# Optimization experiments

Measured on AMD Instinct MI355X. Metric: run time of the kernel, lower is better.

Reference implementation:

```python
import jax, jax.numpy as jnp
import numpy as np

B, N1, N2, D, L, H = 2, 384, 384, 128, 3, 128
DM_MIN = 0.5


def _gat_layer(x, adj, W, Wb, A, gW, gb):
    # GAT_gate from jaechanglim/DTI_PDBbind: attention softmax over dim 1, gated residual
    h = x @ W + Wb                                   # [B,N,D]
    e = jnp.einsum('bjl,bkl->bjk', h @ A, h)
    e = e + jnp.swapaxes(e, 1, 2)
    att = jnp.where(adj > 0, e, -9e15)
    att = jax.nn.softmax(att, axis=1) * adj
    h_prime = jax.nn.relu(jnp.einsum('bij,bjk->bik', att, h))
    coeff = jax.nn.sigmoid(jnp.concatenate([x, h_prime], -1) @ gW + gb)  # [B,N,1]
    return coeff * x + (1.0 - coeff) * h_prime


def _pair_mlp(h1g, h2g, W1, b1, W2, b2):
    # MLP(concat(h1_i, h2_j)) without materializing the [B,N1,N2,2D] concat:
    # split W1 into ligand / protein halves and broadcast-add the projections.
    p1 = jnp.einsum('bnd,dk->bnk', h1g, W1[:D])      # [B,N1,H]
    p2 = jnp.einsum('bmd,dk->bmk', h2g, W1[D:])      # [B,N2,H]
    hid = jax.nn.relu(p1[:, :, None, :] + p2[:, None, :, :] + b1)  # [B,N1,N2,H]
    return (hid @ W2 + b2)[..., 0]                   # [B,N1,N2]


def reference(h1, adj1, h2, dmv, charge1, charge2, vdw_epsilon, vdw_sigma,
              delta_uff, valid1, valid2, no_metal1, no_metal2,
              node_W, gat_W, gat_Wb, gat_A, gat_gW, gat_gb,
              pair_W1, pair_b1, pair_W2, pair_b2,
              vdw_coeff, duff_coeff, int_W1, int_b1, int_W2, int_b2):
    h1g = h1 @ node_W
    h2g = h2 @ node_W
    for i in range(L):  # only ligand graph is convolved (as in the source)
        h1g = _gat_layer(h1g, adj1, gat_W[i], gat_Wb[i], gat_A[i], gat_gW[i], gat_gb[i])

    dm = jnp.sqrt(jnp.sum(dmv * dmv, -1) + 1e-10)    # [B,N1,N2]
    dm = jnp.where(dm < DM_MIN, 1e10, dm)

    # coulomb term (pair MLPs 0,1)
    cA = jax.nn.sigmoid(_pair_mlp(h1g, h2g, pair_W1[0], pair_b1[0], pair_W2[0], pair_b2[0]))
    cN = jax.nn.sigmoid(_pair_mlp(h1g, h2g, pair_W1[1], pair_b1[1], pair_W2[1], pair_b2[1])) * 2.0 + 1.0
    charge12 = charge1[:, :, None] * charge2[:, None, :]
    e_c = cA * charge12 * jnp.power(1.0 / dm, cN)
    e_c = e_c * valid1[:, :, None] * valid2[:, None, :]
    e_c = jnp.clip(e_c, -100.0, 100.0)
    e_c = jnp.sum(e_c, axis=(1, 2))[:, None]

    # vdw term (pair MLPs 2=A sigmoid, 3=B tanh, 4=N sigmoid)
    vA = (jax.nn.sigmoid(_pair_mlp(h1g, h2g, pair_W1[2], pair_b1[2], pair_W2[2], pair_b2[2])) * 0.6 + 0.7)
    vA = vA * (vdw_coeff[0] * vdw_coeff[0]) * vdw_epsilon
    vB = jnp.tanh(_pair_mlp(h1g, h2g, pair_W1[3], pair_b1[3], pair_W2[3], pair_b2[3])) * 0.6 + 0.7
    vN = jax.nn.sigmoid(_pair_mlp(h1g, h2g, pair_W1[4], pair_b1[4], pair_W2[4], pair_b2[4])) * 2.0 + 5.0
    dm0 = vdw_sigma * vB
    dm0 = jnp.where(dm0 < 1e-4, 1.0, dm0)
    r = jnp.power(dm0 / dm, vN)
    e_v = vA * (r * r - 2.0 * r)                     # (dm0/dm)^(2N) - 2(dm0/dm)^N
    e_v = e_v * no_metal1[:, :, None] * no_metal2[:, None, :]
    e_v = jnp.minimum(e_v, 100.0)
    e_v = jnp.sum(e_v, axis=(1, 2))[:, None]

    # conformational energy difference term
    e_u = (duff_coeff[0] * duff_coeff[0] * delta_uff)[:, None]

    # learned intercept from pooled ligand features
    hs = jnp.sum(h1g * valid1[..., None], axis=1)
    inter = jax.nn.relu(hs @ int_W1 + int_b1) @ int_W2 + int_b2

    return jnp.concatenate([e_c, e_v, e_u, inter], -1)  # [B,4]


def setup_inputs() -> dict:
    key = jax.random.key(0)
    ks = jax.random.split(key, 24)
    inp = {}
    inp['h1'] = jax.random.normal(ks[0], (B, N1, 54), jnp.float32)
    inp['h2'] = jax.random.normal(ks[1], (B, N2, 54), jnp.float32)
    a = jax.random.uniform(ks[2], (B, N1, N1))
    adj = (a > 0.9).astype(jnp.float32)
    adj = jnp.maximum(adj, jnp.swapaxes(adj, 1, 2))
    inp['adj1'] = jnp.maximum(adj, jnp.eye(N1, dtype=jnp.float32)[None])
    inp['dmv'] = jax.random.normal(ks[3], (B, N1, N2, 3), jnp.float32) * 3.0
    inp['charge1'] = jax.random.normal(ks[4], (B, N1), jnp.float32) * 0.3
    inp['charge2'] = jax.random.normal(ks[5], (B, N2), jnp.float32) * 0.3
    inp['vdw_epsilon'] = jax.random.uniform(ks[6], (B, N1, N2), jnp.float32) * 0.3
    inp['vdw_sigma'] = 3.0 + jax.random.uniform(ks[7], (B, N1, N2), jnp.float32)
    inp['delta_uff'] = jax.random.uniform(ks[8], (B,), jnp.float32) * 5.0
    inp['valid1'] = jnp.ones((B, N1), jnp.float32)
    inp['valid2'] = jnp.ones((B, N2), jnp.float32)
    inp['no_metal1'] = jnp.ones((B, N1), jnp.float32)
    inp['no_metal2'] = jnp.ones((B, N2), jnp.float32)
    # parameters
    inp['node_W'] = jax.random.normal(ks[9], (54, D), jnp.float32) * 0.1
    inp['gat_W'] = jax.random.normal(ks[10], (L, D, D), jnp.float32) * (1.0 / np.sqrt(D))
    inp['gat_Wb'] = jnp.zeros((L, D), jnp.float32)
    inp['gat_A'] = jax.random.normal(ks[11], (L, D, D), jnp.float32) * 0.05
    inp['gat_gW'] = jax.random.normal(ks[12], (L, 2 * D, 1), jnp.float32) * 0.05
    inp['gat_gb'] = jnp.zeros((L, 1), jnp.float32)
    inp['pair_W1'] = jax.random.normal(ks[13], (5, 2 * D, H), jnp.float32) * 0.05
    inp['pair_b1'] = jnp.zeros((5, H), jnp.float32)
    inp['pair_W2'] = jax.random.normal(ks[14], (5, H, 1), jnp.float32) * 0.1
    inp['pair_b2'] = jnp.zeros((5, 1), jnp.float32)
    inp['vdw_coeff'] = jnp.array([0.02], jnp.float32)
    inp['duff_coeff'] = jnp.array([0.1], jnp.float32)
    inp['int_W1'] = jax.random.normal(ks[15], (D, H), jnp.float32) * 0.05
    inp['int_b1'] = jnp.zeros((H,), jnp.float32)
    inp['int_W2'] = jax.random.normal(ks[16], (H, 1), jnp.float32) * 0.1
    inp['int_b2'] = jnp.zeros((1,), jnp.float32)
    return inp
```

## Files before the change

### kernel.cpp

```cpp
#include <hip/hip_runtime.h>
#include <math.h>

#define BB 2
#define NN 384
#define DD 128
#define HH 128
#define RT_ALL (BB * NN)
#define PCOLS (BB * NN)

__device__ __forceinline__ float sigmoidf_(float x) { return 1.f / (1.f + __expf(-x)); }
__device__ __forceinline__ float tanhf_(float x)    { return 1.f - 2.f / (__expf(2.f * x) + 1.f); }

__global__ __launch_bounds__(256) void k_embed(
    const float* __restrict__ h1, const float* __restrict__ h2,
    const float* __restrict__ nW, float* __restrict__ h1g, float* __restrict__ h2g) {
  int r0 = blockIdx.x * 2;
  int tid = threadIdx.x;
  const float* src; float* dst; int rb;
  if (r0 < RT_ALL) { src = h1; dst = h1g; rb = r0; }
  else             { src = h2; dst = h2g; rb = r0 - RT_ALL; }
  __shared__ float xs[2][54];
  if (tid < 108) xs[tid / 54][tid % 54] = src[rb * 54 + tid];
  __syncthreads();
  int rr = tid >> 7, c = tid & 127;
  float acc = 0.f;
#pragma unroll 6
  for (int k = 0; k < 54; ++k) acc += xs[rr][k] * nW[k * DD + c];
  dst[(rb + rr) * DD + c] = acc;
}

__global__ __launch_bounds__(256) void k_gat_hhA(
    const float* __restrict__ x, const float* __restrict__ W,
    const float* __restrict__ Wb, const float* __restrict__ A,
    float* __restrict__ h, float* __restrict__ hA,
    float* __restrict__ hT, float* __restrict__ hAT) {
  int r = blockIdx.x;
  int tid = threadIdx.x, c = tid & 127, kh = tid >> 7;
  __shared__ float xs[DD], hs[DD];
  __shared__ float ph[2][DD];
  if (tid < DD) xs[tid] = x[r * DD + tid];
  __syncthreads();
  float acc = 0.f;
  const float* Wp = W + (kh * 64) * DD + c;
#pragma unroll 4
  for (int k = 0; k < 64; ++k) acc += xs[kh * 64 + k] * Wp[k * DD];
  ph[kh][c] = acc;
  __syncthreads();
  if (tid < DD) {
    float hv = ph[0][tid] + ph[1][tid] + Wb[tid];
    h[r * DD + tid] = hv; hT[tid * PCOLS + r] = hv; hs[tid] = hv;
  }
  __syncthreads();
  acc = 0.f;
  const float* Ap = A + (kh * 64) * DD + c;
#pragma unroll 4
  for (int k = 0; k < 64; ++k) acc += hs[kh * 64 + k] * Ap[k * DD];
  ph[kh][c] = acc;
  __syncthreads();
  if (tid < DD) {
    float av = ph[0][tid] + ph[1][tid];
    hA[r * DD + tid] = av; hAT[tid * PCOLS + r] = av;
  }
}

__global__ __launch_bounds__(384) void k_gat_att(
    const float* __restrict__ h, const float* __restrict__ hA,
    const float* __restrict__ hT, const float* __restrict__ hAT,
    const float* __restrict__ adj, float* __restrict__ attT) {
  int col = blockIdx.x;
  int b = col / NN;
  int tid = threadIdx.x;
  const float* hrow  = h  + col * DD;
  const float* hArow = hA + col * DD;
  const float* hTb  = hT  + b * NN + tid;
  const float* hATb = hAT + b * NN + tid;
  float e = 0.f;
#pragma unroll 8
  for (int c = 0; c < DD; ++c)
    e += hATb[c * PCOLS] * hrow[c] + hTb[c * PCOLS] * hArow[c];
  float a = adj[col * NN + tid];
  __shared__ float rmx[6], rsm[6];
  float lmax = (a > 0.f) ? e : -3e38f;
#pragma unroll
  for (int off = 32; off > 0; off >>= 1) lmax = fmaxf(lmax, __shfl_down(lmax, off));
  if ((tid & 63) == 0) rmx[tid >> 6] = lmax;
  __syncthreads();
  float m = fmaxf(fmaxf(fmaxf(rmx[0], rmx[1]), fmaxf(rmx[2], rmx[3])), fmaxf(rmx[4], rmx[5]));
  float v = (a > 0.f) ? __expf(e - m) : 0.f;
  float s = v;
#pragma unroll
  for (int off = 32; off > 0; off >>= 1) s += __shfl_down(s, off);
  if ((tid & 63) == 0) rsm[tid >> 6] = s;
  __syncthreads();
  float inv = 1.f / (rsm[0] + rsm[1] + rsm[2] + rsm[3] + rsm[4] + rsm[5]);
  attT[col * NN + tid] = v * a * inv;
}

__global__ __launch_bounds__(256) void k_gat_out(
    const float* __restrict__ x, const float* __restrict__ h,
    const float* __restrict__ attT, const float* __restrict__ gW,
    const float* __restrict__ gb, float* __restrict__ out) {
  int r = blockIdx.x;
  int b = r / NN, i = r - b * NN;
  int tid = threadIdx.x, c = tid & 127, jh = tid >> 7;
  __shared__ float arow[NN];
  __shared__ float ph[2][DD];
  __shared__ float redw[2];
  for (int idx = tid; idx < NN; idx += 256) arow[idx] = attT[(b * NN + idx) * NN + i];
  __syncthreads();
  float acc = 0.f;
  const float* hp = h + (b * NN + jh * 192) * DD + c;
#pragma unroll 4
  for (int jj = 0; jj < 192; ++jj) acc += arow[jh * 192 + jj] * hp[jj * DD];
  ph[jh][c] = acc;
  __syncthreads();
  if (tid < DD) {
    float hpr = fmaxf(ph[0][tid] + ph[1][tid], 0.f);
    float xr = x[r * DD + tid];
    float v = xr * gW[tid] + hpr * gW[DD + tid];
#pragma unroll
    for (int off = 32; off > 0; off >>= 1) v += __shfl_down(v, off);
    if ((tid & 63) == 0) redw[tid >> 6] = v;
  }
  __syncthreads();
  if (tid < DD) {
    float hpr = fmaxf(ph[0][tid] + ph[1][tid], 0.f);
    float xr = x[r * DD + tid];
    float coeff = sigmoidf_(redw[0] + redw[1] + gb[0]);
    out[r * DD + tid] = coeff * xr + (1.f - coeff) * hpr;
  }
}

__global__ __launch_bounds__(256) void k_pair_proj(
    const float* __restrict__ h1g, const float* __restrict__ h2g,
    const float* __restrict__ W1, const float* __restrict__ b1,
    const float* __restrict__ delta_uff, const float* __restrict__ duff_coeff,
    float* __restrict__ p1, float* __restrict__ p2T, float* __restrict__ out) {
  const int RT = 16;
  int m = blockIdx.x % 5;
  int r0 = (blockIdx.x / 5) * RT;
  int tid = threadIdx.x, c = tid & 127, kh = tid >> 7;
  if (blockIdx.x == 0 && tid < BB * 4) {
    int bb = tid >> 2, cc = tid & 3;
    out[tid] = (cc == 2) ? duff_coeff[0] * duff_coeff[0] * delta_uff[bb] : 0.f;
  }
  bool lig = (r0 < RT_ALL);
  const float* src = lig ? h1g : h2g;
  int rb = lig ? r0 : r0 - RT_ALL;
  const float* W = W1 + (m * 256 + (lig ? 0 : 128)) * HH;
  __shared__ float xs[RT][DD];
  __shared__ float ps[RT][DD];
  for (int idx = tid; idx < RT * DD; idx += 256) xs[idx >> 7][idx & 127] = src[rb * DD + idx];
  __syncthreads();
  float acc[RT];
#pragma unroll
  for (int r = 0; r < RT; ++r) acc[r] = 0.f;
  const float* Wp = W + (kh * 64) * HH + c;
#pragma unroll 2
  for (int k = 0; k < 64; ++k) {
    float w = Wp[k * HH];
#pragma unroll
    for (int r = 0; r < RT; ++r) acc[r] += xs[r][kh * 64 + k] * w;
  }
  if (kh == 1) {
#pragma unroll
    for (int r = 0; r < RT; ++r) ps[r][c] = acc[r];
  }
  __syncthreads();
  if (kh == 0) {
    if (lig) {
      float bias = b1[m * HH + c];
#pragma unroll
      for (int r = 0; r < RT; ++r)
        p1[((rb + r) * 5 + m) * HH + c] = acc[r] + ps[r][c] + bias;
    } else {
      float* dst = p2T + (m * HH + c) * PCOLS + rb;
#pragma unroll
      for (int q = 0; q < RT / 4; ++q) {
        float4 v = make_float4(acc[4 * q + 0] + ps[4 * q + 0][c],
                               acc[4 * q + 1] + ps[4 * q + 1][c],
                               acc[4 * q + 2] + ps[4 * q + 2][c],
                               acc[4 * q + 3] + ps[4 * q + 3][c]);
        *(float4*)(dst + 4 * q) = v;
      }
    }
  }
}

__global__ __launch_bounds__(192) void k_pair_energy(
    const float* __restrict__ p1, const float* __restrict__ p2T,
    const float* __restrict__ W2, const float* __restrict__ b2,
    const float* __restrict__ dmv, const float* __restrict__ charge1,
    const float* __restrict__ charge2, const float* __restrict__ veps,
    const float* __restrict__ vsig, const float* __restrict__ valid1,
    const float* __restrict__ valid2, const float* __restrict__ nm1,
    const float* __restrict__ nm2, const float* __restrict__ vdw_coeff,
    const float* __restrict__ h1g, float* __restrict__ ws_int,
    float* __restrict__ out) {
  int tid = threadIdx.x;
  if (blockIdx.x >= 768) {
    int eb = blockIdx.x - 768;
    int b = eb >> 2, ch = eb & 3;
    if (tid < DD) {
      float acc = 0.f;
      int i0 = ch * 96;
#pragma unroll 4
      for (int i = 0; i < 96; ++i) {
        int gi = b * NN + i0 + i;
        acc += h1g[gi * DD + tid] * valid1[gi];
      }
      ws_int[eb * DD + tid] = acc;
    }
    return;
  }
  const int TI = 2;
  int tile = blockIdx.x >> 1, jh = blockIdx.x & 1;
  int r0 = tile * TI;
  int b = r0 / NN;
  int j = jh * 192 + tid;
  int col = b * NN + j;

  const float* q0 = p1 + (r0 + 0) * 5 * HH;
  const float* q1 = p1 + (r0 + 1) * 5 * HH;
  float acc0[5], acc1[5];
#pragma unroll
  for (int m = 0; m < 5; ++m) {
    const float* p2c = p2T + m * HH * PCOLS + col;
    const float* w2m = W2 + m * HH;
    const float* x0 = q0 + m * HH;
    const float* x1 = q1 + m * HH;
    float a0 = b2[m], a1 = b2[m];
#pragma unroll 8
    for (int h = 0; h < HH; ++h) {
      float pv = p2c[h * PCOLS];
      float w = w2m[h];
      a0 += fmaxf(x0[h] + pv, 0.f) * w;
      a1 += fmaxf(x1[h] + pv, 0.f) * w;
    }
    acc0[m] = a0; acc1[m] = a1;
  }

  float q2c = charge2[col], v2 = valid2[col], n2 = nm2[col];
  float vc2 = vdw_coeff[0] * vdw_coeff[0];
  float ec_sum = 0.f, ev_sum = 0.f;
#pragma unroll
  for (int ti = 0; ti < TI; ++ti) {
    const float* am = ti ? acc1 : acc0;
    int gi = r0 + ti;
    int pidx = gi * NN + j;
    float dx = dmv[pidx * 3 + 0], dy = dmv[pidx * 3 + 1], dz = dmv[pidx * 3 + 2];
    float dm = sqrtf(dx * dx + dy * dy + dz * dz + 1e-10f);
    if (dm < 0.5f) dm = 1e10f;
    float cA = sigmoidf_(am[0]);
    float cN = sigmoidf_(am[1]) * 2.f + 1.f;
    float e_c = cA * charge1[gi] * q2c * __powf(1.f / dm, cN);
    e_c *= valid1[gi] * v2;
    e_c = fminf(fmaxf(e_c, -100.f), 100.f);
    ec_sum += e_c;
    float vA = (sigmoidf_(am[2]) * 0.6f + 0.7f) * vc2 * veps[pidx];
    float vB = tanhf_(am[3]) * 0.6f + 0.7f;
    float vN = sigmoidf_(am[4]) * 2.f + 5.f;
    float dm0 = vsig[pidx] * vB;
    if (dm0 < 1e-4f) dm0 = 1.f;
    float rr = __powf(dm0 / dm, vN);
    float e_v = vA * (rr * rr - 2.f * rr);
    e_v *= nm1[gi] * n2;
    e_v = fminf(e_v, 100.f);
    ev_sum += e_v;
  }
#pragma unroll
  for (int off = 32; off > 0; off >>= 1) {
    ec_sum += __shfl_down(ec_sum, off);
    ev_sum += __shfl_down(ev_sum, off);
  }
  __shared__ float rec[3], rev[3];
  if ((tid & 63) == 0) { rec[tid >> 6] = ec_sum; rev[tid >> 6] = ev_sum; }
  __syncthreads();
  if (tid == 0) {
    atomicAdd(&out[b * 4 + 0], rec[0] + rec[1] + rec[2]);
    atomicAdd(&out[b * 4 + 1], rev[0] + rev[1] + rev[2]);
  }
}

__global__ __launch_bounds__(256) void k_intercept_fin(
    const float* __restrict__ ws_int, const float* __restrict__ W1,
    const float* __restrict__ b1, const float* __restrict__ W2,
    const float* __restrict__ b2, float* __restrict__ out) {
  int b = blockIdx.x;
  int tid = threadIdx.x, c = tid & 127, kh = tid >> 7;
  __shared__ float hsf[DD];
  __shared__ float ph[2][DD];
  __shared__ float redw[2];
  if (tid < DD)
    hsf[tid] = ws_int[(b * 4 + 0) * DD + tid] + ws_int[(b * 4 + 1) * DD + tid]
             + ws_int[(b * 4 + 2) * DD + tid] + ws_int[(b * 4 + 3) * DD + tid];
  __syncthreads();
  float acc = 0.f;
  const float* Wp = W1 + (kh * 64) * HH + c;
#pragma unroll 4
  for (int k = 0; k < 64; ++k) acc += hsf[kh * 64 + k] * Wp[k * HH];
  ph[kh][c] = acc;
  __syncthreads();
  if (tid < DD) {
    float hid = fmaxf(ph[0][tid] + ph[1][tid] + b1[tid], 0.f);
    float v = hid * W2[tid];
#pragma unroll
    for (int off = 32; off > 0; off >>= 1) v += __shfl_down(v, off);
    if ((tid & 63) == 0) redw[tid >> 6] = v;
  }
  __syncthreads();
  if (tid == 0) out[b * 4 + 3] = redw[0] + redw[1] + b2[0];
}

extern "C" void kernel_launch(void* const* d_in, const int* in_sizes, int n_in,
                              void* d_out, int out_size, void* d_ws, size_t ws_size,
                              hipStream_t stream) {
  (void)in_sizes; (void)n_in; (void)out_size; (void)ws_size;
  const float* h1         = (const float*)d_in[0];
  const float* h2         = (const float*)d_in[1];
  const float* adj1       = (const float*)d_in[2];
  const float* dmv        = (const float*)d_in[3];
  const float* charge1    = (const float*)d_in[4];
  const float* charge2    = (const float*)d_in[5];
  const float* veps       = (const float*)d_in[6];
  const float* vsig       = (const float*)d_in[7];
  const float* delta_uff  = (const float*)d_in[8];
  const float* valid1     = (const float*)d_in[9];
  const float* valid2     = (const float*)d_in[10];
  const float* nm1        = (const float*)d_in[11];
  const float* nm2        = (const float*)d_in[12];
  const float* node_W     = (const float*)d_in[13];
  const float* gat_W      = (const float*)d_in[14];
  const float* gat_Wb     = (const float*)d_in[15];
  const float* gat_A      = (const float*)d_in[16];
  const float* gat_gW     = (const float*)d_in[17];
  const float* gat_gb     = (const float*)d_in[18];
  const float* pW1        = (const float*)d_in[19];
  const float* pb1        = (const float*)d_in[20];
  const float* pW2        = (const float*)d_in[21];
  const float* pb2        = (const float*)d_in[22];
  const float* vdw_coeff  = (const float*)d_in[23];
  const float* duff_coeff = (const float*)d_in[24];
  const float* iW1        = (const float*)d_in[25];
  const float* ib1        = (const float*)d_in[26];
  const float* iW2        = (const float*)d_in[27];
  const float* ib2        = (const float*)d_in[28];
  float* out = (float*)d_out;

  float* ws = (float*)d_ws;
  const int RN = BB * NN * DD;
  float* h1gA   = ws;
  float* h1gB   = h1gA + RN;
  float* h2g    = h1gB + RN;
  float* hbuf   = h2g + RN;
  float* hAbuf  = hbuf + RN;
  float* hTbuf  = hAbuf + RN;
  float* hATbuf = hTbuf + RN;
  float* attT   = hATbuf + RN;
  float* p1     = attT + BB * NN * NN;
  float* p2T    = p1 + BB * NN * 5 * HH;
  float* ws_int = p2T + 5 * HH * PCOLS;

  k_embed<<<dim3(2 * BB * NN / 2), dim3(256), 0, stream>>>(h1, h2, node_W, h1gA, h2g);

  float* cur = h1gA;
  float* nxt = h1gB;
  for (int l = 0; l < 3; ++l) {
    k_gat_hhA<<<dim3(BB * NN), dim3(256), 0, stream>>>(
        cur, gat_W + l * DD * DD, gat_Wb + l * DD, gat_A + l * DD * DD,
        hbuf, hAbuf, hTbuf, hATbuf);
    k_gat_att<<<dim3(BB * NN), dim3(384), 0, stream>>>(
        hbuf, hAbuf, hTbuf, hATbuf, adj1, attT);
    k_gat_out<<<dim3(BB * NN), dim3(256), 0, stream>>>(
        cur, hbuf, attT, gat_gW + l * 2 * DD, gat_gb + l, nxt);
    float* t = cur; cur = nxt; nxt = t;
  }
  const float* h1gF = cur;

  k_pair_proj<<<dim3((2 * BB * NN / 16) * 5), dim3(256), 0, stream>>>(
      h1gF, h2g, pW1, pb1, delta_uff, duff_coeff, p1, p2T, out);
  k_pair_energy<<<dim3(768 + 8), dim3(192), 0, stream>>>(
      p1, p2T, pW2, pb2, dmv, charge1, charge2, veps, vsig,
      valid1, valid2, nm1, nm2, vdw_coeff, h1gF, ws_int, out);
  k_intercept_fin<<<dim3(BB), dim3(256), 0, stream>>>(ws_int, iW1, ib1, iW2, ib2, out);
}
```

Measured before the change: 325.7 us.

## Vectorize pair-energy loads with float4-interleaved p2 and shared p1/W2 staging

The p2 projection is stored as groups of four hidden units interleaved per column, so the pair-energy kernel reads float4 per step, and the p1 rows and W2 are staged in shared memory instead of being read through global pointers. The GAT attention kernel now writes the attention matrix untransposed, with a strided scatter, so the output kernel can read its row contiguously with float4 loads. The output kernel also splits its accumulation into two chains, and the attention kernel stages its h and hA rows in shared memory. These changes cut global load instructions and strided gathers in the hot loops, at the cost of uncoalesced scattered stores in the attention and projection kernels.

```diff
diff --git a/kernel.cpp b/kernel.cpp
--- a/kernel.cpp
+++ b/kernel.cpp
@@ -66,20 +66,22 @@
 __global__ __launch_bounds__(384) void k_gat_att(
     const float* __restrict__ h, const float* __restrict__ hA,
     const float* __restrict__ hT, const float* __restrict__ hAT,
-    const float* __restrict__ adj, float* __restrict__ attT) {
+    const float* __restrict__ adj, float* __restrict__ att) {
   int col = blockIdx.x;
-  int b = col / NN;
+  int b = col / NN, k = col - b * NN;
   int tid = threadIdx.x;
-  const float* hrow  = h  + col * DD;
-  const float* hArow = hA + col * DD;
+  __shared__ float hrow_s[DD], hArow_s[DD];
+  __shared__ float rmx[6], rsm[6];
+  if (tid < DD) hrow_s[tid] = h[col * DD + tid];
+  else if (tid < 2 * DD) hArow_s[tid - DD] = hA[col * DD + tid - DD];
+  __syncthreads();
   const float* hTb  = hT  + b * NN + tid;
   const float* hATb = hAT + b * NN + tid;
   float e = 0.f;
 #pragma unroll 8
   for (int c = 0; c < DD; ++c)
-    e += hATb[c * PCOLS] * hrow[c] + hTb[c * PCOLS] * hArow[c];
+    e += hATb[c * PCOLS] * hrow_s[c] + hTb[c * PCOLS] * hArow_s[c];
   float a = adj[col * NN + tid];
-  __shared__ float rmx[6], rsm[6];
   float lmax = (a > 0.f) ? e : -3e38f;
 #pragma unroll
   for (int off = 32; off > 0; off >>= 1) lmax = fmaxf(lmax, __shfl_down(lmax, off));
@@ -93,26 +95,30 @@
   if ((tid & 63) == 0) rsm[tid >> 6] = s;
   __syncthreads();
   float inv = 1.f / (rsm[0] + rsm[1] + rsm[2] + rsm[3] + rsm[4] + rsm[5]);
-  attT[col * NN + tid] = v * a * inv;
+  att[(b * NN + tid) * NN + k] = v * a * inv;
 }
 
 __global__ __launch_bounds__(256) void k_gat_out(
     const float* __restrict__ x, const float* __restrict__ h,
-    const float* __restrict__ attT, const float* __restrict__ gW,
+    const float* __restrict__ att, const float* __restrict__ gW,
     const float* __restrict__ gb, float* __restrict__ out) {
   int r = blockIdx.x;
-  int b = r / NN, i = r - b * NN;
+  int b = r / NN;
   int tid = threadIdx.x, c = tid & 127, jh = tid >> 7;
   __shared__ float arow[NN];
   __shared__ float ph[2][DD];
   __shared__ float redw[2];
-  for (int idx = tid; idx < NN; idx += 256) arow[idx] = attT[(b * NN + idx) * NN + i];
-  __syncthreads();
-  float acc = 0.f;
+  if (tid < 96) ((float4*)arow)[tid] = ((const float4*)(att + r * NN))[tid];
+  __syncthreads();
+  float accA = 0.f, accB = 0.f;
   const float* hp = h + (b * NN + jh * 192) * DD + c;
-#pragma unroll 4
-  for (int jj = 0; jj < 192; ++jj) acc += arow[jh * 192 + jj] * hp[jj * DD];
-  ph[jh][c] = acc;
+  const float* ar = arow + jh * 192;
+#pragma unroll 4
+  for (int jj = 0; jj < 192; jj += 2) {
+    accA += ar[jj] * hp[jj * DD];
+    accB += ar[jj + 1] * hp[(jj + 1) * DD];
+  }
+  ph[jh][c] = accA + accB;
   __syncthreads();
   if (tid < DD) {
     float hpr = fmaxf(ph[0][tid] + ph[1][tid], 0.f);
@@ -135,7 +141,7 @@
     const float* __restrict__ h1g, const float* __restrict__ h2g,
     const float* __restrict__ W1, const float* __restrict__ b1,
     const float* __restrict__ delta_uff, const float* __restrict__ duff_coeff,
-    float* __restrict__ p1, float* __restrict__ p2T, float* __restrict__ out) {
+    float* __restrict__ p1, float* __restrict__ p2q, float* __restrict__ out) {
   const int RT = 16;
   int m = blockIdx.x % 5;
   int r0 = (blockIdx.x / 5) * RT;
@@ -174,21 +180,16 @@
       for (int r = 0; r < RT; ++r)
         p1[((rb + r) * 5 + m) * HH + c] = acc[r] + ps[r][c] + bias;
     } else {
-      float* dst = p2T + (m * HH + c) * PCOLS + rb;
-#pragma unroll
-      for (int q = 0; q < RT / 4; ++q) {
-        float4 v = make_float4(acc[4 * q + 0] + ps[4 * q + 0][c],
-                               acc[4 * q + 1] + ps[4 * q + 1][c],
-                               acc[4 * q + 2] + ps[4 * q + 2][c],
-                               acc[4 * q + 3] + ps[4 * q + 3][c]);
-        *(float4*)(dst + 4 * q) = v;
-      }
+      int g = m * (HH / 4) + (c >> 2);
+      float* dst = p2q + (size_t)(g * PCOLS + rb) * 4 + (c & 3);
+#pragma unroll
+      for (int r = 0; r < RT; ++r) dst[4 * r] = acc[r] + ps[r][c];
     }
   }
 }
 
 __global__ __launch_bounds__(192) void k_pair_energy(
-    const float* __restrict__ p1, const float* __restrict__ p2T,
+    const float* __restrict__ p1, const float* __restrict__ p2q,
     const float* __restrict__ W2, const float* __restrict__ b2,
     const float* __restrict__ dmv, const float* __restrict__ charge1,
     const float* __restrict__ charge2, const float* __restrict__ veps,
@@ -220,24 +221,33 @@
   int j = jh * 192 + tid;
   int col = b * NN + j;
 
-  const float* q0 = p1 + (r0 + 0) * 5 * HH;
-  const float* q1 = p1 + (r0 + 1) * 5 * HH;
+  __shared__ float4 p1s4[2][5 * HH / 4];
+  __shared__ float4 w2s4[5 * HH / 4];
+  {
+    const float4* p1g = (const float4*)(p1 + r0 * 5 * HH);
+    for (int idx = tid; idx < 2 * 160; idx += 192) p1s4[idx / 160][idx % 160] = p1g[idx];
+    if (tid < 160) w2s4[tid] = ((const float4*)W2)[tid];
+  }
+  __syncthreads();
+
+  const float4* p2q4 = (const float4*)p2q;
   float acc0[5], acc1[5];
 #pragma unroll
   for (int m = 0; m < 5; ++m) {
-    const float* p2c = p2T + m * HH * PCOLS + col;
-    const float* w2m = W2 + m * HH;
-    const float* x0 = q0 + m * HH;
-    const float* x1 = q1 + m * HH;
-    float a0 = b2[m], a1 = b2[m];
+    const float4* pc = p2q4 + (size_t)(m * 32) * PCOLS + col;
+    float a0 = 0.f, a1 = 0.f;
 #pragma unroll 8
-    for (int h = 0; h < HH; ++h) {
-      float pv = p2c[h * PCOLS];
-      float w = w2m[h];
-      a0 += fmaxf(x0[h] + pv, 0.f) * w;
-      a1 += fmaxf(x1[h] + pv, 0.f) * w;
+    for (int hq = 0; hq < 32; ++hq) {
+      float4 pv = pc[(size_t)hq * PCOLS];
+      float4 x0 = p1s4[0][m * 32 + hq];
+      float4 x1 = p1s4[1][m * 32 + hq];
+      float4 w  = w2s4[m * 32 + hq];
+      a0 += fmaxf(x0.x + pv.x, 0.f) * w.x + fmaxf(x0.y + pv.y, 0.f) * w.y
+          + fmaxf(x0.z + pv.z, 0.f) * w.z + fmaxf(x0.w + pv.w, 0.f) * w.w;
+      a1 += fmaxf(x1.x + pv.x, 0.f) * w.x + fmaxf(x1.y + pv.y, 0.f) * w.y
+          + fmaxf(x1.z + pv.z, 0.f) * w.z + fmaxf(x1.w + pv.w, 0.f) * w.w;
     }
-    acc0[m] = a0; acc1[m] = a1;
+    acc0[m] = a0 + b2[m]; acc1[m] = a1 + b2[m];
   }
 
   float q2c = charge2[col], v2 = valid2[col], n2 = nm2[col];
@@ -356,10 +366,10 @@
   float* hAbuf  = hbuf + RN;
   float* hTbuf  = hAbuf + RN;
   float* hATbuf = hTbuf + RN;
-  float* attT   = hATbuf + RN;
-  float* p1     = attT + BB * NN * NN;
-  float* p2T    = p1 + BB * NN * 5 * HH;
-  float* ws_int = p2T + 5 * HH * PCOLS;
+  float* att    = hATbuf + RN;
+  float* p1     = att + BB * NN * NN;
+  float* p2q    = p1 + BB * NN * 5 * HH;
+  float* ws_int = p2q + 5 * HH * PCOLS;
 
   k_embed<<<dim3(2 * BB * NN / 2), dim3(256), 0, stream>>>(h1, h2, node_W, h1gA, h2g);
 
@@ -370,17 +380,17 @@
         cur, gat_W + l * DD * DD, gat_Wb + l * DD, gat_A + l * DD * DD,
         hbuf, hAbuf, hTbuf, hATbuf);
     k_gat_att<<<dim3(BB * NN), dim3(384), 0, stream>>>(
-        hbuf, hAbuf, hTbuf, hATbuf, adj1, attT);
+        hbuf, hAbuf, hTbuf, hATbuf, adj1, att);
     k_gat_out<<<dim3(BB * NN), dim3(256), 0, stream>>>(
-        cur, hbuf, attT, gat_gW + l * 2 * DD, gat_gb + l, nxt);
+        cur, hbuf, att, gat_gW + l * 2 * DD, gat_gb + l, nxt);
     float* t = cur; cur = nxt; nxt = t;
   }
   const float* h1gF = cur;
 
   k_pair_proj<<<dim3((2 * BB * NN / 16) * 5), dim3(256), 0, stream>>>(
-      h1gF, h2g, pW1, pb1, delta_uff, duff_coeff, p1, p2T, out);
+      h1gF, h2g, pW1, pb1, delta_uff, duff_coeff, p1, p2q, out);
   k_pair_energy<<<dim3(768 + 8), dim3(192), 0, stream>>>(
-      p1, p2T, pW2, pb2, dmv, charge1, charge2, veps, vsig,
+      p1, p2q, pW2, pb2, dmv, charge1, charge2, veps, vsig,
       valid1, valid2, nm1, nm2, vdw_coeff, h1gF, ws_int, out);
   k_intercept_fin<<<dim3(BB), dim3(256), 0, stream>>>(ws_int, iW1, ib1, iW2, ib2, out);
 }
```

Result: faster. 316.2 us (-2.9%).
